# Performance work log

Measured on AMD Instinct MI355X. Metric: run time of the kernel, lower is better.

The kernel has to match this reference:

```python
import jax, jax.numpy as jnp
import numpy as np
from functools import partial

STRIDES = (8, 16, 32)
FMP = ((256, 256), (128, 128), (64, 64))  # H, W per level (img 2048, strides 8/16/32)
A = 3          # anchors per cell
C = 80         # num classes
TOPK = 1000    # per-level top-k
CONF = 0.05
NMS_T = 0.6
IMG = 2048.0   # max(img_h, img_w)
OFFSET = 1.0e5 # per-class box offset so cross-class IoU == 0

ANCHOR_SIZE = np.array([[[10, 13], [16, 30], [33, 23]],
                        [[30, 61], [62, 45], [59, 119]],
                        [[116, 90], [156, 198], [373, 326]]], np.float32)


def setup_inputs() -> dict:
    key = jax.random.key(0)
    ks = jax.random.split(key, 9)
    inp = {}
    for lvl, (h, w) in enumerate(FMP):
        m = h * w * A
        inp[f"obj{lvl}"] = jax.random.normal(ks[3 * lvl + 0], (m, 1), jnp.float32)
        inp[f"cls{lvl}"] = jax.random.normal(ks[3 * lvl + 1], (m, C), jnp.float32)
        inp[f"reg{lvl}"] = jax.random.normal(ks[3 * lvl + 2], (m, 4), jnp.float32)
    inp["anchor_size"] = jnp.asarray(ANCHOR_SIZE)
    return inp


def make_anchors(h, w, stride, a_size):
    # a_size: [A, 2]. Matches generate_anchors (cell centers * stride, tiled anchor wh).
    ys, xs = jnp.meshgrid(jnp.arange(h), jnp.arange(w), indexing="ij")
    xy = jnp.stack([xs, ys], -1).reshape(-1, 2).astype(jnp.float32) + 0.5  # [HW, 2]
    xy = jnp.repeat(xy, A, axis=0) * stride                                # [HW*A, 2]
    wh = jnp.tile(a_size, (h * w, 1))                                      # [HW*A, 2]
    return xy, wh


def decode_boxes(axy, awh, reg, stride):
    ctr = axy + (jax.nn.sigmoid(reg[..., :2]) * 3.0 - 1.5) * stride
    wh = jnp.exp(reg[..., 2:]) * awh
    return jnp.concatenate([ctr - 0.5 * wh, ctr + 0.5 * wh], axis=-1)


def iou_matrix(b):
    # b: [N, 4] xyxy
    area = (b[:, 2] - b[:, 0]) * (b[:, 3] - b[:, 1])
    lt = jnp.maximum(b[:, None, :2], b[None, :, :2])
    rb = jnp.minimum(b[:, None, 2:], b[None, :, 2:])
    whi = jnp.clip(rb - lt, 0.0)
    inter = whi[..., 0] * whi[..., 1]
    return inter / (area[:, None] + area[None, :] - inter + 1e-12)


def _post_process(levels, anchor_size):
    all_s, all_l, all_b = [], [], []
    for lvl, (obj, cls, reg) in enumerate(levels):
        h, w = FMP[lvl]
        stride = float(STRIDES[lvl])
        axy, awh = make_anchors(h, w, stride, anchor_size[lvl])
        # joint score, flattened over anchors x classes  -> [M*C]
        scores = jnp.sqrt(jax.nn.sigmoid(obj) * jax.nn.sigmoid(cls)).reshape(-1)
        topk_scores, topk_idx = jax.lax.top_k(scores, TOPK)
        anchor_idx = topk_idx // C
        labels = topk_idx % C
        boxes = decode_boxes(axy[anchor_idx], awh[anchor_idx], reg[anchor_idx], stride)
        # conf filter done by zeroing scores (fixed shapes under jit)
        topk_scores = jnp.where(topk_scores > CONF, topk_scores, 0.0)
        all_s.append(topk_scores); all_l.append(labels); all_b.append(boxes)
    scores = jnp.concatenate(all_s)   # [3*TOPK]
    labels = jnp.concatenate(all_l)
    boxes = jnp.concatenate(all_b)    # [3*TOPK, 4]

    n = scores.shape[0]
    # per-class NMS via class offset (cross-class IoU = 0), greedy over score order
    obox = boxes + labels.astype(boxes.dtype)[:, None] * OFFSET
    order = jnp.argsort(-scores)
    scores_s, labels_s, boxes_s = scores[order], labels[order], boxes[order]
    iou = iou_matrix(obox[order])

    def step(supp, i):
        keep_i = jnp.logical_and(~supp[i], scores_s[i] > CONF)
        supp = supp | (keep_i & (iou[i] > NMS_T) & (jnp.arange(n) > i))
        return supp, keep_i

    _, keep = jax.lax.scan(step, jnp.zeros(n, bool), jnp.arange(n))

    boxes_out = jnp.clip(boxes_s / IMG, 0.0, 1.0)
    scores_out = scores_s * keep.astype(scores_s.dtype)  # suppressed -> score 0
    return boxes_out, scores_out, labels_s


@jax.jit
def reference(obj0, cls0, reg0, obj1, cls1, reg1, obj2, cls2, reg2, anchor_size):
    levels = [(obj0, cls0, reg0), (obj1, cls1, reg1), (obj2, cls2, reg2)]
    return _post_process(levels, anchor_size)
```

## Files before the change

kernel.cpp:

```cpp
#include <hip/hip_runtime.h>
#include <stdint.h>
#include <math.h>

#pragma clang fp contract(off)

typedef unsigned int u32;
typedef unsigned long long u64;

#define M0 196608
#define M1 49152
#define M2 12288
#define MTOT (M0 + M1 + M2)
#define QCAP 8192
#define CCAP 524288
#define SCAP 2048
#define NSEL 3000
#define MASKW 48
#define NCH 47
#define FLOOR_BITS 0x3F4CCCCDu

__device__ __forceinline__ float sigf(float x) { return 1.0f / (1.0f + expf(-x)); }
__device__ __forceinline__ float sig_cr(float x) {
  float e = (float)exp(-(double)x);
  return 1.0f / (1.0f + e);
}

__device__ __forceinline__ void lvlmap(int b, int& lvl, u32& base, int& aoff) {
  if (b < 960)       { lvl = 0; base = (u32)b * 4096u;          aoff = 0; }
  else if (b < 1200) { lvl = 1; base = (u32)(b - 960) * 4096u;  aoff = M0; }
  else               { lvl = 2; base = (u32)(b - 1200) * 4096u; aoff = M0 + M1; }
}

__global__ void ksig_init(const float* __restrict__ o0, const float* __restrict__ o1,
                          const float* __restrict__ o2, float2* __restrict__ sopair,
                          u32* __restrict__ ghist, u32* __restrict__ qcnt,
                          u64* __restrict__ okbits, u64* __restrict__ nzbits) {
  int g = blockIdx.x * 256 + threadIdx.x;
  if (g < 6144) ghist[g] = 0u;
  if (g < 8) qcnt[g] = 0u;
  if (g < 64) { okbits[g] = 0ull; nzbits[g] = 0ull; }
  if (g >= MTOT) return;
  float x = (g < M0) ? o0[g] : (g < M0 + M1 ? o1[g - M0] : o2[g - M0 - M1]);
  float so = sigf(x);
  float tc;
  if (so <= 0.64f) tc = 3.0e38f;
  else {
    float r = 0.64f / so;
    tc = logf(r / (1.0f - r)) - 0.01f;
  }
  sopair[g] = make_float2(so, tc);
}

__global__ __launch_bounds__(256) void khist2(
    const float4* __restrict__ cls0, const float4* __restrict__ cls1,
    const float4* __restrict__ cls2, const float2* __restrict__ sopair,
    u32* __restrict__ ghist, u64* __restrict__ cand, u32* __restrict__ qcnt) {
  __shared__ u32 hist[2048];
  __shared__ u64 stage[SCAP];
  __shared__ u32 scount, gbase;
  int tid = threadIdx.x;
  for (int i = tid; i < 2048; i += 256) hist[i] = 0u;
  if (tid == 0) scount = 0u;
  __syncthreads();
  int lvl, aoff; u32 base;
  lvlmap(blockIdx.x, lvl, base, aoff);
  const float4* cls = lvl == 0 ? cls0 : (lvl == 1 ? cls1 : cls2);
#pragma unroll 4
  for (int c = 0; c < 16; c++) {
    u32 f4i = base + (u32)(c * 256 + tid);
    float4 v = cls[f4i];
    float2 sp = sopair[aoff + (int)(f4i / 20u)];
    float xs[4] = {v.x, v.y, v.z, v.w};
#pragma unroll
    for (int k = 0; k < 4; k++) {
      if (xs[k] >= sp.y) {
        u32 bits = __float_as_uint(sqrtf(sp.x * sigf(xs[k])));
        if (bits >= FLOOR_BITS) {
          atomicAdd(&hist[(bits - 0x3F000000u) >> 12], 1u);
          u32 sp_ = atomicAdd(&scount, 1u);
          if (sp_ < SCAP) {
            u32 idx = f4i * 4u + (u32)k;
            stage[sp_] = ((u64)__float_as_uint(xs[k]) << 32) |
                         ((u64)lvl << 24) | (u64)idx;
          }
        }
      }
    }
  }
  __syncthreads();
  u32 n = scount; if (n > SCAP) n = SCAP;
  if (tid == 0) {
    gbase = atomicAdd(&qcnt[3], n);
    if (scount > SCAP) atomicOr(&qcnt[4], 1u);
  }
  __syncthreads();
  u32 gb = gbase;
  for (u32 i = tid; i < n; i += 256) {
    u32 gp = gb + i;
    if (gp < CCAP) cand[gp] = stage[i];
    else if (i == 0) atomicOr(&qcnt[4], 1u);
  }
  for (int i = tid; i < 2048; i += 256) {
    u32 h = hist[i];
    if (h) atomicAdd(&ghist[lvl * 2048 + i], h);
  }
}

__global__ void kthresh(const u32* __restrict__ ghist, u32* __restrict__ thresh) {
  __shared__ u32 A[2048], Bb[2048];
  int lvl = blockIdx.x, tid = threadIdx.x;
  for (int i = tid; i < 2048; i += 256) A[i] = ghist[lvl * 2048 + i];
  __syncthreads();
  u32 *src = A, *dst = Bb;
  for (int off = 1; off < 2048; off <<= 1) {
    for (int i = tid; i < 2048; i += 256)
      dst[i] = src[i] + ((i + off < 2048) ? src[i + off] : 0u);
    __syncthreads();
    u32* t = src; src = dst; dst = t;
  }
  if (tid == 0 && src[0] < 1000u) thresh[lvl] = FLOOR_BITS;
  for (int i = tid; i < 2048; i += 256) {
    u32 S = src[i];
    u32 Sn = (i < 2047) ? src[i + 1] : 0u;
    if (S >= 1000u && Sn < 1000u) {
      u32 th = 0x3F000000u + ((u32)i << 12);
      thresh[lvl] = (th >= 0x3F000000u + 1024u) ? th - 1024u : 0x3F000000u;
    }
  }
}

__global__ __launch_bounds__(256) void kfilter(
    const u64* __restrict__ cand, const float2* __restrict__ sopair,
    const float* __restrict__ obj0, const float* __restrict__ obj1,
    const float* __restrict__ obj2, const u32* __restrict__ thresh,
    u32* __restrict__ qsc, u32* __restrict__ qidx, u32* __restrict__ qcnt) {
  if (qcnt[4] != 0u) return;
  u32 cnt = qcnt[3]; if (cnt > CCAP) cnt = CCAP;
  for (u32 i = blockIdx.x * 256u + threadIdx.x; i < cnt; i += 256u * 256u) {
    u64 e = cand[i];
    float clsv = __uint_as_float((u32)(e >> 32));
    u32 lo = (u32)e;
    int lvl = (int)((lo >> 24) & 3u);
    u32 idx = lo & 0xFFFFFFu;
    u32 anchor = idx / 80u;
    int aoff = lvl == 0 ? 0 : (lvl == 1 ? M0 : M0 + M1);
    float so = sopair[aoff + (int)anchor].x;
    u32 bits = __float_as_uint(sqrtf(so * sigf(clsv)));
    if (bits >= thresh[lvl]) {
      const float* obj = lvl == 0 ? obj0 : (lvl == 1 ? obj1 : obj2);
      float s = sqrtf(sig_cr(obj[anchor]) * sig_cr(clsv));
      u32 qp = atomicAdd(&qcnt[lvl], 1u);
      if (qp < QCAP) {
        qsc[lvl * QCAP + qp] = __float_as_uint(s);
        qidx[lvl * QCAP + qp] = idx;
      }
    }
  }
}

__global__ __launch_bounds__(256) void kqual_fb(
    const float4* __restrict__ cls0, const float4* __restrict__ cls1,
    const float4* __restrict__ cls2, const float2* __restrict__ sopair,
    const float* __restrict__ obj0, const float* __restrict__ obj1,
    const float* __restrict__ obj2, const u32* __restrict__ thresh,
    u32* __restrict__ qsc, u32* __restrict__ qidx, u32* __restrict__ qcnt) {
  if (qcnt[4] == 0u) return;
  int lvl, aoff; u32 base;
  lvlmap(blockIdx.x, lvl, base, aoff);
  const float4* cls = lvl == 0 ? cls0 : (lvl == 1 ? cls1 : cls2);
  const float* obj = lvl == 0 ? obj0 : (lvl == 1 ? obj1 : obj2);
  u32 th = thresh[lvl];
  int tid = threadIdx.x;
  for (int c = 0; c < 16; c++) {
    u32 f4i = base + (u32)(c * 256 + tid);
    float4 v = cls[f4i];
    float2 sp = sopair[aoff + (int)(f4i / 20u)];
    float xs[4] = {v.x, v.y, v.z, v.w};
#pragma unroll
    for (int k = 0; k < 4; k++) {
      if (xs[k] >= sp.y) {
        u32 bits = __float_as_uint(sqrtf(sp.x * sigf(xs[k])));
        if (bits >= th) {
          u32 idx = f4i * 4u + (u32)k;
          u32 anchor = idx / 80u;
          float s = sqrtf(sig_cr(obj[anchor]) * sig_cr(xs[k]));
          u32 qp = atomicAdd(&qcnt[lvl], 1u);
          if (qp < QCAP) {
            qsc[lvl * QCAP + qp] = __float_as_uint(s);
            qidx[lvl * QCAP + qp] = idx;
          }
        }
      }
    }
  }
}

__global__ __launch_bounds__(256) void krank(
    const u32* __restrict__ qsc, const u32* __restrict__ qidx,
    const u32* __restrict__ qcnt,
    const float4* __restrict__ reg0, const float4* __restrict__ reg1,
    const float4* __restrict__ reg2, const float* __restrict__ asz,
    u32* __restrict__ label_u, float4* __restrict__ box_u,
    float* __restrict__ lscore) {
  __shared__ u32 kb[2048];
  __shared__ u32 ki[2048];
  int lvl = blockIdx.x >> 5;
  int t = (blockIdx.x & 31) * 256 + threadIdx.x;
  u32 qn = qcnt[lvl]; if (qn > QCAP) qn = QCAP;
  u32 mb = 0, mi = 0; bool has = t < (int)qn;
  if (has) { mb = qsc[lvl * QCAP + t]; mi = qidx[lvl * QCAP + t]; }
  u32 rank = 0;
  for (u32 b0 = 0; b0 < qn; b0 += 2048u) {
    u32 m = qn - b0; if (m > 2048u) m = 2048u;
    u32 mpad = (m + 7u) & ~7u;
    __syncthreads();
    for (u32 j = threadIdx.x; j < mpad; j += 256) {
      if (j < m) { kb[j] = qsc[lvl * QCAP + b0 + j]; ki[j] = qidx[lvl * QCAP + b0 + j]; }
      else       { kb[j] = 0u; ki[j] = 0xFFFFFFFFu; }
    }
    __syncthreads();
    if (has) {
      u32 r0 = 0, r1 = 0, r2 = 0, r3 = 0;
      for (u32 j = 0; j < mpad; j += 8) {
        u32 a0 = kb[j+0], a1 = kb[j+1], a2 = kb[j+2], a3 = kb[j+3];
        u32 a4 = kb[j+4], a5 = kb[j+5], a6 = kb[j+6], a7 = kb[j+7];
        u32 i0 = ki[j+0], i1 = ki[j+1], i2 = ki[j+2], i3 = ki[j+3];
        u32 i4 = ki[j+4], i5 = ki[j+5], i6 = ki[j+6], i7 = ki[j+7];
        r0 += (a0 > mb || (a0 == mb && i0 < mi)) ? 1u : 0u;
        r1 += (a1 > mb || (a1 == mb && i1 < mi)) ? 1u : 0u;
        r2 += (a2 > mb || (a2 == mb && i2 < mi)) ? 1u : 0u;
        r3 += (a3 > mb || (a3 == mb && i3 < mi)) ? 1u : 0u;
        r0 += (a4 > mb || (a4 == mb && i4 < mi)) ? 1u : 0u;
        r1 += (a5 > mb || (a5 == mb && i5 < mi)) ? 1u : 0u;
        r2 += (a6 > mb || (a6 == mb && i6 < mi)) ? 1u : 0u;
        r3 += (a7 > mb || (a7 == mb && i7 < mi)) ? 1u : 0u;
      }
      rank += r0 + r1 + r2 + r3;
    }
  }
  if (!has || rank >= 1000u) return;

  int p = lvl * 1000 + (int)rank;
  u32 idx = mi;
  u32 anchor = idx / 80u;
  u32 label = idx - anchor * 80u;
  u32 cell = anchor / 3u;
  u32 a = anchor - cell * 3u;
  int W = 256 >> lvl;
  u32 x = cell & (u32)(W - 1);
  u32 y = cell >> (8 - lvl);
  float stride = (float)(8 << lvl);
  float ax = ((float)x + 0.5f) * stride;
  float ay = ((float)y + 0.5f) * stride;
  const float4* reg = lvl == 0 ? reg0 : (lvl == 1 ? reg1 : reg2);
  float4 rg = reg[anchor];
  float aw = asz[lvl * 6 + (int)a * 2 + 0];
  float ah = asz[lvl * 6 + (int)a * 2 + 1];
  float cx = ax + (sigf(rg.x) * 3.0f - 1.5f) * stride;
  float cy = ay + (sigf(rg.y) * 3.0f - 1.5f) * stride;
  float bw = expf(rg.z) * aw;
  float bh = expf(rg.w) * ah;
  box_u[p] = make_float4(cx - 0.5f * bw, cy - 0.5f * bh, cx + 0.5f * bw, cy + 0.5f * bh);
  label_u[p] = label;
  float sv = __uint_as_float(mb);
  lscore[p] = (sv > 0.05f) ? sv : 0.0f;
}

__device__ __forceinline__ u32 cnt_ge(const float* A, float s) {
  u32 lo = 0, hi = 1000;
  while (lo < hi) { u32 mid = (lo + hi) >> 1; if (A[mid] >= s) lo = mid + 1; else hi = mid; }
  return lo;
}
__device__ __forceinline__ u32 cnt_gt(const float* A, float s) {
  u32 lo = 0, hi = 1000;
  while (lo < hi) { u32 mid = (lo + hi) >> 1; if (A[mid] > s) lo = mid + 1; else hi = mid; }
  return lo;
}

__global__ __launch_bounds__(256) void kmerge(const float* __restrict__ lscore,
                                              const u32* __restrict__ label_u,
                                              const float4* __restrict__ box_u,
                                              float* __restrict__ sscore,
                                              float4* __restrict__ obox,
                                              u64* __restrict__ okbits,
                                              float* __restrict__ out) {
  __shared__ float s0[1000], s1[1000], s2[1000];
  int tid = threadIdx.x;
  for (int j = tid; j < 1000; j += 256) {
    s0[j] = lscore[j]; s1[j] = lscore[1000 + j]; s2[j] = lscore[2000 + j];
  }
  __syncthreads();
  int p = blockIdx.x * 256 + tid;
  if (p >= NSEL) return;
  int lvl = p / 1000, r = p - lvl * 1000;
  float s = lvl == 0 ? s0[r] : (lvl == 1 ? s1[r] : s2[r]);
  u32 rank = (u32)r;
  if (lvl == 0)      rank += cnt_gt(s1, s) + cnt_gt(s2, s);
  else if (lvl == 1) rank += cnt_ge(s0, s) + cnt_gt(s2, s);
  else               rank += cnt_ge(s0, s) + cnt_ge(s1, s);

  u32 label = label_u[p];
  float4 bx = box_u[p];
  sscore[rank] = s;
  float off = (float)label * 1.0e5f;
  obox[rank] = make_float4(bx.x + off, bx.y + off, bx.z + off, bx.w + off);
  out[rank * 4 + 0] = fminf(fmaxf(bx.x / 2048.0f, 0.0f), 1.0f);
  out[rank * 4 + 1] = fminf(fmaxf(bx.y / 2048.0f, 0.0f), 1.0f);
  out[rank * 4 + 2] = fminf(fmaxf(bx.z / 2048.0f, 0.0f), 1.0f);
  out[rank * 4 + 3] = fminf(fmaxf(bx.w / 2048.0f, 0.0f), 1.0f);
  out[15000 + rank] = (float)label;
  if (s > 0.05f) atomicOr(&okbits[rank >> 6], 1ull << (rank & 63));
}

__global__ __launch_bounds__(256) void kiou(const float4* __restrict__ obox,
                                            u64* __restrict__ mask,
                                            u64* __restrict__ diag,
                                            u64* __restrict__ nzbits) {
  __shared__ u32 crossflags;
  int tid = threadIdx.x;
  if (tid == 0) crossflags = 0u;
  __syncthreads();
  int i0 = blockIdx.x * 4;
  float4 b0v = obox[i0 + 0], b1v = obox[i0 + 1], b2v = obox[i0 + 2], b3v = obox[i0 + 3];
  float a0 = (b0v.z - b0v.x) * (b0v.w - b0v.y);
  float a1 = (b1v.z - b1v.x) * (b1v.w - b1v.y);
  float a2 = (b2v.z - b2v.x) * (b2v.w - b2v.y);
  float a3 = (b3v.z - b3v.x) * (b3v.w - b3v.y);
  bool c0 = false, c1 = false, c2 = false, c3 = false;
  for (int it = 0; it < 12; it++) {
    int jj = it * 256 + tid;
    int jc = jj < NSEL ? jj : NSEL - 1;
    float4 bj = obox[jc];
    float aj = (bj.z - bj.x) * (bj.w - bj.y);
    int wi = it * 4 + (tid >> 6);
#define DOROW(R, BV, AV, CV) do {                                              \
      float ltx = fmaxf(BV.x, bj.x), lty = fmaxf(BV.y, bj.y);                  \
      float rbx = fminf(BV.z, bj.z), rby = fminf(BV.w, bj.w);                  \
      float ww = fmaxf(rbx - ltx, 0.0f), hh = fmaxf(rby - lty, 0.0f);          \
      float inter = ww * hh;                                                   \
      float iou = inter / (((AV + aj) - inter) + 1e-12f);                      \
      bool cond = (jj < NSEL) && (jj > (i0 + R)) && (iou > 0.6f);              \
      CV |= (cond && wi != ((i0 + R) >> 6));                                   \
      u64 m = __ballot(cond);                                                  \
      if ((tid & 63) == 0) {                                                   \
        mask[(u64)(i0 + R) * MASKW + (u64)wi] = m;                             \
        if (wi == ((i0 + R) >> 6)) diag[i0 + R] = m;                           \
      }                                                                        \
    } while (0)
    DOROW(0, b0v, a0, c0); DOROW(1, b1v, a1, c1);
    DOROW(2, b2v, a2, c2); DOROW(3, b3v, a3, c3);
#undef DOROW
  }
  u64 bb;
  bb = __ballot(c0); if ((tid & 63) == 0 && bb) atomicOr(&crossflags, 1u);
  bb = __ballot(c1); if ((tid & 63) == 0 && bb) atomicOr(&crossflags, 2u);
  bb = __ballot(c2); if ((tid & 63) == 0 && bb) atomicOr(&crossflags, 4u);
  bb = __ballot(c3); if ((tid & 63) == 0 && bb) atomicOr(&crossflags, 8u);
  __syncthreads();
  if (tid < 4 && ((crossflags >> tid) & 1u))
    atomicOr(&nzbits[(i0 + tid) >> 6], 1ull << ((i0 + tid) & 63));
}

__global__ __launch_bounds__(64) void knms(const u64* __restrict__ mask,
                                           const u64* __restrict__ diag,
                                           const u64* __restrict__ okbits,
                                           const u64* __restrict__ nzbits,
                                           const float* __restrict__ sscore,
                                           float* __restrict__ out) {
  __shared__ u64 sdiag[NCH * 64];
  __shared__ float ssc[NCH * 64];
  int l = threadIdx.x;
  for (int i = l; i < NCH * 64; i += 64) {
    sdiag[i] = (i < NSEL) ? diag[i] : 0ull;
    ssc[i]   = (i < NSEL) ? sscore[i] : 0.0f;
  }
  u64 okw_l = (l < NCH) ? okbits[l] : 0ull;
  u64 nz_l  = (l < NCH) ? nzbits[l] : 0ull;
  u64 supp = 0ull;
  __syncthreads();
  for (int c = 0; c < NCH; c++) {
    int base = c * 64;
    u64 cur = __shfl(supp, c);
    u64 okw = __shfl(okw_l, c);
    u64 nzw = __shfl(nz_l, c);
    u64 dj = sdiag[base + l];
    u64 diagnz = __ballot(dj != 0ull);
    u64 avail = okw & ~cur;
    u64 isupp = 0ull, procd = 0ull, tent = avail;
    while (true) {
      tent = avail & ~isupp;
      u64 evs = tent & diagnz & ~procd;
      if (evs == 0ull) break;
      int j = __ffsll((long long)evs) - 1;
      procd |= (1ull << j);
      isupp |= __shfl(dj, j);
    }
    u64 kept = tent;
    int row = base + l;
    if (row < NSEL) out[12000 + row] = ((kept >> l) & 1ull) ? ssc[row] : 0.0f;
    u64 orrows = kept & nzw;
    while (orrows) {
      int j = __ffsll((long long)orrows) - 1;
      orrows &= orrows - 1ull;
      u64 w = (l < NCH) ? mask[(u64)(base + j) * MASKW + l] : 0ull;
      supp |= w;
    }
  }
}

extern "C" void kernel_launch(void* const* d_in, const int* in_sizes, int n_in,
                              void* d_out, int out_size, void* d_ws, size_t ws_size,
                              hipStream_t stream) {
  const float* obj0 = (const float*)d_in[0];
  const float* cls0 = (const float*)d_in[1];
  const float* reg0 = (const float*)d_in[2];
  const float* obj1 = (const float*)d_in[3];
  const float* cls1 = (const float*)d_in[4];
  const float* reg1 = (const float*)d_in[5];
  const float* obj2 = (const float*)d_in[6];
  const float* cls2 = (const float*)d_in[7];
  const float* reg2 = (const float*)d_in[8];
  const float* asz  = (const float*)d_in[9];
  float* out = (float*)d_out;

  char* wsp = (char*)d_ws;
  size_t off = 0;
  auto alloc = [&](size_t bytes) -> void* {
    void* p = wsp + off;
    off += (bytes + 255) & ~(size_t)255;
    return p;
  };
  float2* sopair = (float2*)alloc((size_t)MTOT * 8);
  u32* ghist   = (u32*)alloc((size_t)3 * 2048 * 4);
  u32* qcnt    = (u32*)alloc(64);
  u32* thresh  = (u32*)alloc(64);
  u64* cand    = (u64*)alloc((size_t)CCAP * 8);
  u32* qsc     = (u32*)alloc((size_t)3 * QCAP * 4);
  u32* qidx    = (u32*)alloc((size_t)3 * QCAP * 4);
  u32* label_u = (u32*)alloc((size_t)NSEL * 4);
  float4* box_u  = (float4*)alloc((size_t)NSEL * 16);
  float* lscore  = (float*)alloc((size_t)NSEL * 4);
  float4* obox   = (float4*)alloc((size_t)NSEL * 16);
  float* sscore  = (float*)alloc((size_t)NSEL * 4);
  u64* okbits    = (u64*)alloc(64 * 8);
  u64* nzbits    = (u64*)alloc(64 * 8);
  u64* diag      = (u64*)alloc((size_t)NSEL * 8);
  u64* mask      = (u64*)alloc((size_t)NSEL * MASKW * 8);
  if (off > ws_size) return;

  ksig_init<<<dim3(1008), dim3(256), 0, stream>>>(obj0, obj1, obj2, sopair,
                                                  ghist, qcnt, okbits, nzbits);
  khist2<<<dim3(1260), dim3(256), 0, stream>>>((const float4*)cls0, (const float4*)cls1,
                                               (const float4*)cls2, sopair, ghist,
                                               cand, qcnt);
  kthresh<<<dim3(3), dim3(256), 0, stream>>>(ghist, thresh);
  kfilter<<<dim3(256), dim3(256), 0, stream>>>(cand, sopair, obj0, obj1, obj2,
                                               thresh, qsc, qidx, qcnt);
  kqual_fb<<<dim3(1260), dim3(256), 0, stream>>>((const float4*)cls0, (const float4*)cls1,
                                                 (const float4*)cls2, sopair,
                                                 obj0, obj1, obj2, thresh,
                                                 qsc, qidx, qcnt);
  krank<<<dim3(96), dim3(256), 0, stream>>>(qsc, qidx, qcnt, (const float4*)reg0,
                                            (const float4*)reg1, (const float4*)reg2,
                                            asz, label_u, box_u, lscore);
  kmerge<<<dim3(12), dim3(256), 0, stream>>>(lscore, label_u, box_u, sscore, obox,
                                             okbits, out);
  kiou<<<dim3(750), dim3(256), 0, stream>>>(obox, mask, diag, nzbits);
  knms<<<dim3(1), dim3(64), 0, stream>>>(mask, diag, okbits, nzbits, sscore, out);
}
```

Baseline: 280.5 us.

## Fuse post-histogram stages into one cooperative kernel and drop sigmoid precompute

Replaces the sequence of small tail kernels (threshold, filter, fallback, rank, merge, IoU, NMS) with a single cooperative kernel that uses grid-wide syncs between phases. The objectness-sigmoid precompute kernel is removed by computing per-anchor sigmoid and threshold in shared memory inside the histogram kernel, which also gains a per-float4 max early-out. Candidates now store score bits instead of raw logits. Workspace clearing moves to a memset. The aim is to cut launch gaps and the extra global pass, at the cost of grid-sync overhead and a fixed 256-block tail.

```diff
diff --git a/kernel.cpp b/kernel.cpp
--- a/kernel.cpp
+++ b/kernel.cpp
@@ -1,8 +1,11 @@
 #include <hip/hip_runtime.h>
+#include <hip/hip_cooperative_groups.h>
 #include <stdint.h>
 #include <math.h>
 
 #pragma clang fp contract(off)
+
+namespace cg = cooperative_groups;
 
 typedef unsigned int u32;
 typedef unsigned long long u64;
@@ -10,14 +13,16 @@
 #define M0 196608
 #define M1 49152
 #define M2 12288
-#define MTOT (M0 + M1 + M2)
 #define QCAP 8192
 #define CCAP 524288
-#define SCAP 2048
+#define SCAP 1024
+#define FSTG 256
 #define NSEL 3000
 #define MASKW 48
 #define NCH 47
 #define FLOOR_BITS 0x3F4CCCCDu
+#define NBLK_H 2520
+#define TBLK 256
 
 __device__ __forceinline__ float sigf(float x) { return 1.0f / (1.0f + expf(-x)); }
 __device__ __forceinline__ float sig_cr(float x) {
@@ -25,63 +30,59 @@
   return 1.0f / (1.0f + e);
 }
 
-__device__ __forceinline__ void lvlmap(int b, int& lvl, u32& base, int& aoff) {
-  if (b < 960)       { lvl = 0; base = (u32)b * 4096u;          aoff = 0; }
-  else if (b < 1200) { lvl = 1; base = (u32)(b - 960) * 4096u;  aoff = M0; }
-  else               { lvl = 2; base = (u32)(b - 1200) * 4096u; aoff = M0 + M1; }
-}
-
-__global__ void ksig_init(const float* __restrict__ o0, const float* __restrict__ o1,
-                          const float* __restrict__ o2, float2* __restrict__ sopair,
-                          u32* __restrict__ ghist, u32* __restrict__ qcnt,
-                          u64* __restrict__ okbits, u64* __restrict__ nzbits) {
-  int g = blockIdx.x * 256 + threadIdx.x;
-  if (g < 6144) ghist[g] = 0u;
-  if (g < 8) qcnt[g] = 0u;
-  if (g < 64) { okbits[g] = 0ull; nzbits[g] = 0ull; }
-  if (g >= MTOT) return;
-  float x = (g < M0) ? o0[g] : (g < M0 + M1 ? o1[g - M0] : o2[g - M0 - M1]);
-  float so = sigf(x);
-  float tc;
-  if (so <= 0.64f) tc = 3.0e38f;
-  else {
-    float r = 0.64f / so;
-    tc = logf(r / (1.0f - r)) - 0.01f;
-  }
-  sopair[g] = make_float2(so, tc);
+__device__ __forceinline__ void lvlmap2(int b, int& lvl, u32& base) {
+  if (b < 1920)      { lvl = 0; base = (u32)b * 2048u; }
+  else if (b < 2400) { lvl = 1; base = (u32)(b - 1920) * 2048u; }
+  else               { lvl = 2; base = (u32)(b - 2400) * 2048u; }
 }
 
 __global__ __launch_bounds__(256) void khist2(
     const float4* __restrict__ cls0, const float4* __restrict__ cls1,
-    const float4* __restrict__ cls2, const float2* __restrict__ sopair,
+    const float4* __restrict__ cls2, const float* __restrict__ obj0,
+    const float* __restrict__ obj1, const float* __restrict__ obj2,
     u32* __restrict__ ghist, u64* __restrict__ cand, u32* __restrict__ qcnt) {
   __shared__ u32 hist[2048];
   __shared__ u64 stage[SCAP];
+  __shared__ float sof[112], tcf[112];
   __shared__ u32 scount, gbase;
   int tid = threadIdx.x;
   for (int i = tid; i < 2048; i += 256) hist[i] = 0u;
   if (tid == 0) scount = 0u;
+  int lvl; u32 base;
+  lvlmap2(blockIdx.x, lvl, base);
+  const float4* cls = lvl == 0 ? cls0 : (lvl == 1 ? cls1 : cls2);
+  const float* obj = lvl == 0 ? obj0 : (lvl == 1 ? obj1 : obj2);
+  u32 a0 = base / 20u;
+  u32 na = (base + 2047u) / 20u - a0 + 1u;
+  if (tid < (int)na) {
+    float so = sigf(obj[a0 + tid]);
+    float tc;
+    if (so <= 0.64f) tc = 3.0e38f;
+    else { float r = 0.64f / so; tc = logf(r / (1.0f - r)) - 0.01f; }
+    sof[tid] = so; tcf[tid] = tc;
+  }
   __syncthreads();
-  int lvl, aoff; u32 base;
-  lvlmap(blockIdx.x, lvl, base, aoff);
-  const float4* cls = lvl == 0 ? cls0 : (lvl == 1 ? cls1 : cls2);
-#pragma unroll 4
-  for (int c = 0; c < 16; c++) {
+#pragma unroll 2
+  for (int c = 0; c < 8; c++) {
     u32 f4i = base + (u32)(c * 256 + tid);
     float4 v = cls[f4i];
-    float2 sp = sopair[aoff + (int)(f4i / 20u)];
-    float xs[4] = {v.x, v.y, v.z, v.w};
+    u32 ai = f4i / 20u - a0;
+    float tc = tcf[ai];
+    float mx = fmaxf(fmaxf(v.x, v.y), fmaxf(v.z, v.w));
+    if (mx >= tc) {
+      float so = sof[ai];
+      float xs[4] = {v.x, v.y, v.z, v.w};
 #pragma unroll
-    for (int k = 0; k < 4; k++) {
-      if (xs[k] >= sp.y) {
-        u32 bits = __float_as_uint(sqrtf(sp.x * sigf(xs[k])));
-        if (bits >= FLOOR_BITS) {
-          atomicAdd(&hist[(bits - 0x3F000000u) >> 12], 1u);
-          u32 sp_ = atomicAdd(&scount, 1u);
-          if (sp_ < SCAP) {
-            u32 idx = f4i * 4u + (u32)k;
-            stage[sp_] = ((u64)__float_as_uint(xs[k]) << 32) |
-                         ((u64)lvl << 24) | (u64)idx;
+      for (int k = 0; k < 4; k++) {
+        if (xs[k] >= tc) {
+          u32 bits = __float_as_uint(sqrtf(so * sigf(xs[k])));
+          if (bits >= FLOOR_BITS) {
+            atomicAdd(&hist[(bits - 0x3F000000u) >> 12], 1u);
+            u32 sp = atomicAdd(&scount, 1u);
+            if (sp < SCAP) {
+              u32 idx = f4i * 4u + (u32)k;
+              stage[sp] = ((u64)bits << 32) | ((u64)lvl << 24) | (u64)idx;
+            }
           }
         }
       }
@@ -91,14 +92,13 @@
   u32 n = scount; if (n > SCAP) n = SCAP;
   if (tid == 0) {
     gbase = atomicAdd(&qcnt[3], n);
-    if (scount > SCAP) atomicOr(&qcnt[4], 1u);
+    if (scount > SCAP || gbase + n > CCAP) atomicOr(&qcnt[4], 1u);
   }
   __syncthreads();
   u32 gb = gbase;
   for (u32 i = tid; i < n; i += 256) {
     u32 gp = gb + i;
     if (gp < CCAP) cand[gp] = stage[i];
-    else if (i == 0) atomicOr(&qcnt[4], 1u);
   }
   for (int i = tid; i < 2048; i += 256) {
     u32 h = hist[i];
@@ -106,165 +106,29 @@
   }
 }
 
-__global__ void kthresh(const u32* __restrict__ ghist, u32* __restrict__ thresh) {
-  __shared__ u32 A[2048], Bb[2048];
-  int lvl = blockIdx.x, tid = threadIdx.x;
-  for (int i = tid; i < 2048; i += 256) A[i] = ghist[lvl * 2048 + i];
-  __syncthreads();
-  u32 *src = A, *dst = Bb;
-  for (int off = 1; off < 2048; off <<= 1) {
-    for (int i = tid; i < 2048; i += 256)
-      dst[i] = src[i] + ((i + off < 2048) ? src[i + off] : 0u);
-    __syncthreads();
-    u32* t = src; src = dst; dst = t;
-  }
-  if (tid == 0 && src[0] < 1000u) thresh[lvl] = FLOOR_BITS;
-  for (int i = tid; i < 2048; i += 256) {
-    u32 S = src[i];
-    u32 Sn = (i < 2047) ? src[i + 1] : 0u;
-    if (S >= 1000u && Sn < 1000u) {
-      u32 th = 0x3F000000u + ((u32)i << 12);
-      thresh[lvl] = (th >= 0x3F000000u + 1024u) ? th - 1024u : 0x3F000000u;
-    }
-  }
-}
-
-__global__ __launch_bounds__(256) void kfilter(
-    const u64* __restrict__ cand, const float2* __restrict__ sopair,
-    const float* __restrict__ obj0, const float* __restrict__ obj1,
-    const float* __restrict__ obj2, const u32* __restrict__ thresh,
-    u32* __restrict__ qsc, u32* __restrict__ qidx, u32* __restrict__ qcnt) {
-  if (qcnt[4] != 0u) return;
-  u32 cnt = qcnt[3]; if (cnt > CCAP) cnt = CCAP;
-  for (u32 i = blockIdx.x * 256u + threadIdx.x; i < cnt; i += 256u * 256u) {
-    u64 e = cand[i];
-    float clsv = __uint_as_float((u32)(e >> 32));
-    u32 lo = (u32)e;
-    int lvl = (int)((lo >> 24) & 3u);
-    u32 idx = lo & 0xFFFFFFu;
-    u32 anchor = idx / 80u;
-    int aoff = lvl == 0 ? 0 : (lvl == 1 ? M0 : M0 + M1);
-    float so = sopair[aoff + (int)anchor].x;
-    u32 bits = __float_as_uint(sqrtf(so * sigf(clsv)));
-    if (bits >= thresh[lvl]) {
-      const float* obj = lvl == 0 ? obj0 : (lvl == 1 ? obj1 : obj2);
-      float s = sqrtf(sig_cr(obj[anchor]) * sig_cr(clsv));
-      u32 qp = atomicAdd(&qcnt[lvl], 1u);
-      if (qp < QCAP) {
-        qsc[lvl * QCAP + qp] = __float_as_uint(s);
-        qidx[lvl * QCAP + qp] = idx;
-      }
-    }
-  }
-}
-
-__global__ __launch_bounds__(256) void kqual_fb(
-    const float4* __restrict__ cls0, const float4* __restrict__ cls1,
-    const float4* __restrict__ cls2, const float2* __restrict__ sopair,
-    const float* __restrict__ obj0, const float* __restrict__ obj1,
-    const float* __restrict__ obj2, const u32* __restrict__ thresh,
-    u32* __restrict__ qsc, u32* __restrict__ qidx, u32* __restrict__ qcnt) {
-  if (qcnt[4] == 0u) return;
-  int lvl, aoff; u32 base;
-  lvlmap(blockIdx.x, lvl, base, aoff);
-  const float4* cls = lvl == 0 ? cls0 : (lvl == 1 ? cls1 : cls2);
-  const float* obj = lvl == 0 ? obj0 : (lvl == 1 ? obj1 : obj2);
-  u32 th = thresh[lvl];
-  int tid = threadIdx.x;
-  for (int c = 0; c < 16; c++) {
-    u32 f4i = base + (u32)(c * 256 + tid);
-    float4 v = cls[f4i];
-    float2 sp = sopair[aoff + (int)(f4i / 20u)];
-    float xs[4] = {v.x, v.y, v.z, v.w};
-#pragma unroll
-    for (int k = 0; k < 4; k++) {
-      if (xs[k] >= sp.y) {
-        u32 bits = __float_as_uint(sqrtf(sp.x * sigf(xs[k])));
-        if (bits >= th) {
-          u32 idx = f4i * 4u + (u32)k;
-          u32 anchor = idx / 80u;
-          float s = sqrtf(sig_cr(obj[anchor]) * sig_cr(xs[k]));
-          u32 qp = atomicAdd(&qcnt[lvl], 1u);
-          if (qp < QCAP) {
-            qsc[lvl * QCAP + qp] = __float_as_uint(s);
-            qidx[lvl * QCAP + qp] = idx;
-          }
-        }
-      }
-    }
-  }
-}
-
-__global__ __launch_bounds__(256) void krank(
-    const u32* __restrict__ qsc, const u32* __restrict__ qidx,
-    const u32* __restrict__ qcnt,
-    const float4* __restrict__ reg0, const float4* __restrict__ reg1,
-    const float4* __restrict__ reg2, const float* __restrict__ asz,
-    u32* __restrict__ label_u, float4* __restrict__ box_u,
-    float* __restrict__ lscore) {
-  __shared__ u32 kb[2048];
-  __shared__ u32 ki[2048];
-  int lvl = blockIdx.x >> 5;
-  int t = (blockIdx.x & 31) * 256 + threadIdx.x;
-  u32 qn = qcnt[lvl]; if (qn > QCAP) qn = QCAP;
-  u32 mb = 0, mi = 0; bool has = t < (int)qn;
-  if (has) { mb = qsc[lvl * QCAP + t]; mi = qidx[lvl * QCAP + t]; }
-  u32 rank = 0;
-  for (u32 b0 = 0; b0 < qn; b0 += 2048u) {
-    u32 m = qn - b0; if (m > 2048u) m = 2048u;
-    u32 mpad = (m + 7u) & ~7u;
-    __syncthreads();
-    for (u32 j = threadIdx.x; j < mpad; j += 256) {
-      if (j < m) { kb[j] = qsc[lvl * QCAP + b0 + j]; ki[j] = qidx[lvl * QCAP + b0 + j]; }
-      else       { kb[j] = 0u; ki[j] = 0xFFFFFFFFu; }
-    }
-    __syncthreads();
-    if (has) {
-      u32 r0 = 0, r1 = 0, r2 = 0, r3 = 0;
-      for (u32 j = 0; j < mpad; j += 8) {
-        u32 a0 = kb[j+0], a1 = kb[j+1], a2 = kb[j+2], a3 = kb[j+3];
-        u32 a4 = kb[j+4], a5 = kb[j+5], a6 = kb[j+6], a7 = kb[j+7];
-        u32 i0 = ki[j+0], i1 = ki[j+1], i2 = ki[j+2], i3 = ki[j+3];
-        u32 i4 = ki[j+4], i5 = ki[j+5], i6 = ki[j+6], i7 = ki[j+7];
-        r0 += (a0 > mb || (a0 == mb && i0 < mi)) ? 1u : 0u;
-        r1 += (a1 > mb || (a1 == mb && i1 < mi)) ? 1u : 0u;
-        r2 += (a2 > mb || (a2 == mb && i2 < mi)) ? 1u : 0u;
-        r3 += (a3 > mb || (a3 == mb && i3 < mi)) ? 1u : 0u;
-        r0 += (a4 > mb || (a4 == mb && i4 < mi)) ? 1u : 0u;
-        r1 += (a5 > mb || (a5 == mb && i5 < mi)) ? 1u : 0u;
-        r2 += (a6 > mb || (a6 == mb && i6 < mi)) ? 1u : 0u;
-        r3 += (a7 > mb || (a7 == mb && i7 < mi)) ? 1u : 0u;
-      }
-      rank += r0 + r1 + r2 + r3;
-    }
-  }
-  if (!has || rank >= 1000u) return;
-
-  int p = lvl * 1000 + (int)rank;
-  u32 idx = mi;
-  u32 anchor = idx / 80u;
-  u32 label = idx - anchor * 80u;
-  u32 cell = anchor / 3u;
-  u32 a = anchor - cell * 3u;
-  int W = 256 >> lvl;
-  u32 x = cell & (u32)(W - 1);
-  u32 y = cell >> (8 - lvl);
-  float stride = (float)(8 << lvl);
-  float ax = ((float)x + 0.5f) * stride;
-  float ay = ((float)y + 0.5f) * stride;
-  const float4* reg = lvl == 0 ? reg0 : (lvl == 1 ? reg1 : reg2);
-  float4 rg = reg[anchor];
-  float aw = asz[lvl * 6 + (int)a * 2 + 0];
-  float ah = asz[lvl * 6 + (int)a * 2 + 1];
-  float cx = ax + (sigf(rg.x) * 3.0f - 1.5f) * stride;
-  float cy = ay + (sigf(rg.y) * 3.0f - 1.5f) * stride;
-  float bw = expf(rg.z) * aw;
-  float bh = expf(rg.w) * ah;
-  box_u[p] = make_float4(cx - 0.5f * bw, cy - 0.5f * bh, cx + 0.5f * bw, cy + 0.5f * bh);
-  label_u[p] = label;
-  float sv = __uint_as_float(mb);
-  lscore[p] = (sv > 0.05f) ? sv : 0.0f;
-}
+struct TailArgs {
+  const float *obj0, *obj1, *obj2;
+  const float *cls0f, *cls1f, *cls2f;
+  const float4 *cls0, *cls1, *cls2;
+  const float4 *reg0, *reg1, *reg2;
+  const float *asz;
+  u32 *ghist, *qcnt, *thresh;
+  u64 *cand;
+  u32 *qsc, *qidx, *label_u;
+  float4 *box_u;
+  float *lscore;
+  float4 *obox;
+  float *sscore;
+  u64 *okbits, *nzbits, *diag, *mask;
+  float *out;
+};
+
+struct SmemA { u32 A[2048]; u32 B[2048]; };
+struct SmemB { u32 sc[3][FSTG]; u32 si[3][FSTG]; u32 cnt[3]; u32 gb[3]; };
+struct SmemC { u32 kb[2048]; u32 ki[2048]; };
+struct SmemD { float s0[1000], s1[1000], s2[1000]; u64 okb[NCH]; };
+struct SmemF { u64 sdiag[NCH * 64]; float ssc[NCH * 64]; };
+union TailSmem { SmemA a; SmemB b; SmemC c; SmemD d; SmemF f; };
 
 __device__ __forceinline__ u32 cnt_ge(const float* A, float s) {
   u32 lo = 0, hi = 1000;
@@ -277,133 +141,290 @@
   return lo;
 }
 
-__global__ __launch_bounds__(256) void kmerge(const float* __restrict__ lscore,
-                                              const u32* __restrict__ label_u,
-                                              const float4* __restrict__ box_u,
-                                              float* __restrict__ sscore,
-                                              float4* __restrict__ obox,
-                                              u64* __restrict__ okbits,
-                                              float* __restrict__ out) {
-  __shared__ float s0[1000], s1[1000], s2[1000];
+__global__ __launch_bounds__(256) void ktail(TailArgs ta) {
+  cg::grid_group grid = cg::this_grid();
+  __shared__ TailSmem sm;
+  int bid = blockIdx.x;
   int tid = threadIdx.x;
-  for (int j = tid; j < 1000; j += 256) {
-    s0[j] = lscore[j]; s1[j] = lscore[1000 + j]; s2[j] = lscore[2000 + j];
-  }
-  __syncthreads();
-  int p = blockIdx.x * 256 + tid;
-  if (p >= NSEL) return;
-  int lvl = p / 1000, r = p - lvl * 1000;
-  float s = lvl == 0 ? s0[r] : (lvl == 1 ? s1[r] : s2[r]);
-  u32 rank = (u32)r;
-  if (lvl == 0)      rank += cnt_gt(s1, s) + cnt_gt(s2, s);
-  else if (lvl == 1) rank += cnt_ge(s0, s) + cnt_gt(s2, s);
-  else               rank += cnt_ge(s0, s) + cnt_ge(s1, s);
-
-  u32 label = label_u[p];
-  float4 bx = box_u[p];
-  sscore[rank] = s;
-  float off = (float)label * 1.0e5f;
-  obox[rank] = make_float4(bx.x + off, bx.y + off, bx.z + off, bx.w + off);
-  out[rank * 4 + 0] = fminf(fmaxf(bx.x / 2048.0f, 0.0f), 1.0f);
-  out[rank * 4 + 1] = fminf(fmaxf(bx.y / 2048.0f, 0.0f), 1.0f);
-  out[rank * 4 + 2] = fminf(fmaxf(bx.z / 2048.0f, 0.0f), 1.0f);
-  out[rank * 4 + 3] = fminf(fmaxf(bx.w / 2048.0f, 0.0f), 1.0f);
-  out[15000 + rank] = (float)label;
-  if (s > 0.05f) atomicOr(&okbits[rank >> 6], 1ull << (rank & 63));
-}
-
-__global__ __launch_bounds__(256) void kiou(const float4* __restrict__ obox,
-                                            u64* __restrict__ mask,
-                                            u64* __restrict__ diag,
-                                            u64* __restrict__ nzbits) {
-  __shared__ u32 crossflags;
-  int tid = threadIdx.x;
-  if (tid == 0) crossflags = 0u;
-  __syncthreads();
-  int i0 = blockIdx.x * 4;
-  float4 b0v = obox[i0 + 0], b1v = obox[i0 + 1], b2v = obox[i0 + 2], b3v = obox[i0 + 3];
-  float a0 = (b0v.z - b0v.x) * (b0v.w - b0v.y);
-  float a1 = (b1v.z - b1v.x) * (b1v.w - b1v.y);
-  float a2 = (b2v.z - b2v.x) * (b2v.w - b2v.y);
-  float a3 = (b3v.z - b3v.x) * (b3v.w - b3v.y);
-  bool c0 = false, c1 = false, c2 = false, c3 = false;
-  for (int it = 0; it < 12; it++) {
-    int jj = it * 256 + tid;
-    int jc = jj < NSEL ? jj : NSEL - 1;
-    float4 bj = obox[jc];
-    float aj = (bj.z - bj.x) * (bj.w - bj.y);
-    int wi = it * 4 + (tid >> 6);
+
+  if (bid < 3) {
+    int lvl = bid;
+    if (tid == 0) ta.thresh[lvl] = FLOOR_BITS;
+    for (int i = tid; i < 2048; i += 256) sm.a.A[i] = ta.ghist[lvl * 2048 + i];
+    __syncthreads();
+    u32 *src = sm.a.A, *dst = sm.a.B;
+    for (int off = 1; off < 2048; off <<= 1) {
+      for (int i = tid; i < 2048; i += 256)
+        dst[i] = src[i] + ((i + off < 2048) ? src[i + off] : 0u);
+      __syncthreads();
+      u32* t = src; src = dst; dst = t;
+    }
+    for (int i = tid; i < 2048; i += 256) {
+      u32 S = src[i];
+      u32 Sn = (i < 2047) ? src[i + 1] : 0u;
+      if (S >= 1000u && Sn < 1000u) {
+        u32 th = 0x3F000000u + ((u32)i << 12);
+        ta.thresh[lvl] = (th >= 0x3F000000u + 1024u) ? th - 1024u : 0x3F000000u;
+      }
+    }
+  }
+  grid.sync();
+
+  if (ta.qcnt[4] == 0u) {
+    if (tid < 3) sm.b.cnt[tid] = 0u;
+    __syncthreads();
+    u32 cnt = ta.qcnt[3]; if (cnt > CCAP) cnt = CCAP;
+    u32 th0 = ta.thresh[0], th1 = ta.thresh[1], th2 = ta.thresh[2];
+    for (u32 i = (u32)(bid * 256 + tid); i < cnt; i += (u32)TBLK * 256u) {
+      u64 e = ta.cand[i];
+      u32 bits = (u32)(e >> 32);
+      int lvl = (int)((e >> 24) & 3u);
+      u32 idx = (u32)e & 0xFFFFFFu;
+      u32 th = lvl == 0 ? th0 : (lvl == 1 ? th1 : th2);
+      if (bits >= th) {
+        const float* obj = lvl == 0 ? ta.obj0 : (lvl == 1 ? ta.obj1 : ta.obj2);
+        const float* clsf = lvl == 0 ? ta.cls0f : (lvl == 1 ? ta.cls1f : ta.cls2f);
+        u32 anchor = idx / 80u;
+        float s = sqrtf(sig_cr(obj[anchor]) * sig_cr(clsf[idx]));
+        u32 p = atomicAdd(&sm.b.cnt[lvl], 1u);
+        if (p < FSTG) { sm.b.sc[lvl][p] = __float_as_uint(s); sm.b.si[lvl][p] = idx; }
+        else {
+          u32 qp = atomicAdd(&ta.qcnt[lvl], 1u);
+          if (qp < QCAP) { ta.qsc[lvl * QCAP + qp] = __float_as_uint(s);
+                           ta.qidx[lvl * QCAP + qp] = idx; }
+        }
+      }
+    }
+    __syncthreads();
+    for (int l = 0; l < 3; l++) {
+      u32 n = sm.b.cnt[l]; if (n > FSTG) n = FSTG;
+      if (tid == 0) sm.b.gb[l] = atomicAdd(&ta.qcnt[l], n);
+      __syncthreads();
+      u32 g = sm.b.gb[l];
+      for (u32 i = tid; i < n; i += 256) {
+        u32 qp = g + i;
+        if (qp < QCAP) { ta.qsc[l * QCAP + qp] = sm.b.sc[l][i];
+                         ta.qidx[l * QCAP + qp] = sm.b.si[l][i]; }
+      }
+      __syncthreads();
+    }
+  } else {
+    for (int vb = bid; vb < NBLK_H; vb += TBLK) {
+      int lvl; u32 base;
+      lvlmap2(vb, lvl, base);
+      const float4* cls = lvl == 0 ? ta.cls0 : (lvl == 1 ? ta.cls1 : ta.cls2);
+      const float* obj = lvl == 0 ? ta.obj0 : (lvl == 1 ? ta.obj1 : ta.obj2);
+      u32 th = ta.thresh[lvl];
+      for (int c = 0; c < 8; c++) {
+        u32 f4i = base + (u32)(c * 256 + tid);
+        float4 v = cls[f4i];
+        u32 anchor = f4i / 20u;
+        float so = sigf(obj[anchor]);
+        float xs[4] = {v.x, v.y, v.z, v.w};
+#pragma unroll
+        for (int k = 0; k < 4; k++) {
+          u32 bits = __float_as_uint(sqrtf(so * sigf(xs[k])));
+          if (bits >= th) {
+            u32 idx = f4i * 4u + (u32)k;
+            float s = sqrtf(sig_cr(obj[anchor]) * sig_cr(xs[k]));
+            u32 qp = atomicAdd(&ta.qcnt[lvl], 1u);
+            if (qp < QCAP) { ta.qsc[lvl * QCAP + qp] = __float_as_uint(s);
+                             ta.qidx[lvl * QCAP + qp] = idx; }
+          }
+        }
+      }
+    }
+  }
+  grid.sync();
+
+  if (bid < 96) {
+    int lvl = bid >> 5;
+    int t = (bid & 31) * 256 + tid;
+    u32 qn = ta.qcnt[lvl]; if (qn > QCAP) qn = QCAP;
+    u32 mb = 0, mi = 0; bool has = t < (int)qn;
+    if (has) { mb = ta.qsc[lvl * QCAP + t]; mi = ta.qidx[lvl * QCAP + t]; }
+    u32 rank = 0;
+    for (u32 b0 = 0; b0 < qn; b0 += 2048u) {
+      u32 m = qn - b0; if (m > 2048u) m = 2048u;
+      u32 mpad = (m + 7u) & ~7u;
+      __syncthreads();
+      for (u32 j = tid; j < mpad; j += 256) {
+        if (j < m) { sm.c.kb[j] = ta.qsc[lvl * QCAP + b0 + j];
+                     sm.c.ki[j] = ta.qidx[lvl * QCAP + b0 + j]; }
+        else       { sm.c.kb[j] = 0u; sm.c.ki[j] = 0xFFFFFFFFu; }
+      }
+      __syncthreads();
+      if (has) {
+        u32 r0 = 0, r1 = 0, r2 = 0, r3 = 0;
+        for (u32 j = 0; j < mpad; j += 8) {
+          u32 a0 = sm.c.kb[j+0], a1 = sm.c.kb[j+1], a2 = sm.c.kb[j+2], a3 = sm.c.kb[j+3];
+          u32 a4 = sm.c.kb[j+4], a5 = sm.c.kb[j+5], a6 = sm.c.kb[j+6], a7 = sm.c.kb[j+7];
+          u32 i0 = sm.c.ki[j+0], i1 = sm.c.ki[j+1], i2 = sm.c.ki[j+2], i3 = sm.c.ki[j+3];
+          u32 i4 = sm.c.ki[j+4], i5 = sm.c.ki[j+5], i6 = sm.c.ki[j+6], i7 = sm.c.ki[j+7];
+          r0 += (a0 > mb || (a0 == mb && i0 < mi)) ? 1u : 0u;
+          r1 += (a1 > mb || (a1 == mb && i1 < mi)) ? 1u : 0u;
+          r2 += (a2 > mb || (a2 == mb && i2 < mi)) ? 1u : 0u;
+          r3 += (a3 > mb || (a3 == mb && i3 < mi)) ? 1u : 0u;
+          r0 += (a4 > mb || (a4 == mb && i4 < mi)) ? 1u : 0u;
+          r1 += (a5 > mb || (a5 == mb && i5 < mi)) ? 1u : 0u;
+          r2 += (a6 > mb || (a6 == mb && i6 < mi)) ? 1u : 0u;
+          r3 += (a7 > mb || (a7 == mb && i7 < mi)) ? 1u : 0u;
+        }
+        rank += r0 + r1 + r2 + r3;
+      }
+    }
+    if (has && rank < 1000u) {
+      int p = lvl * 1000 + (int)rank;
+      u32 idx = mi;
+      u32 anchor = idx / 80u;
+      u32 label = idx - anchor * 80u;
+      u32 cell = anchor / 3u;
+      u32 a = anchor - cell * 3u;
+      int W = 256 >> lvl;
+      u32 x = cell & (u32)(W - 1);
+      u32 y = cell >> (8 - lvl);
+      float stride = (float)(8 << lvl);
+      float ax = ((float)x + 0.5f) * stride;
+      float ay = ((float)y + 0.5f) * stride;
+      const float4* reg = lvl == 0 ? ta.reg0 : (lvl == 1 ? ta.reg1 : ta.reg2);
+      float4 rg = reg[anchor];
+      float aw = ta.asz[lvl * 6 + (int)a * 2 + 0];
+      float ah = ta.asz[lvl * 6 + (int)a * 2 + 1];
+      float cx = ax + (sigf(rg.x) * 3.0f - 1.5f) * stride;
+      float cy = ay + (sigf(rg.y) * 3.0f - 1.5f) * stride;
+      float bw = expf(rg.z) * aw;
+      float bh = expf(rg.w) * ah;
+      ta.box_u[p] = make_float4(cx - 0.5f * bw, cy - 0.5f * bh,
+                                cx + 0.5f * bw, cy + 0.5f * bh);
+      ta.label_u[p] = label;
+      float sv = __uint_as_float(mb);
+      ta.lscore[p] = (sv > 0.05f) ? sv : 0.0f;
+    }
+  }
+  grid.sync();
+
+  if (bid < 12) {
+    for (int j = tid; j < 1000; j += 256) {
+      sm.d.s0[j] = ta.lscore[j];
+      sm.d.s1[j] = ta.lscore[1000 + j];
+      sm.d.s2[j] = ta.lscore[2000 + j];
+    }
+    for (int j = tid; j < NCH; j += 256) sm.d.okb[j] = 0ull;
+    __syncthreads();
+    int p = bid * 256 + tid;
+    if (p < NSEL) {
+      int lvl = p / 1000, r = p - lvl * 1000;
+      float s = lvl == 0 ? sm.d.s0[r] : (lvl == 1 ? sm.d.s1[r] : sm.d.s2[r]);
+      u32 rank = (u32)r;
+      if (lvl == 0)      rank += cnt_gt(sm.d.s1, s) + cnt_gt(sm.d.s2, s);
+      else if (lvl == 1) rank += cnt_ge(sm.d.s0, s) + cnt_gt(sm.d.s2, s);
+      else               rank += cnt_ge(sm.d.s0, s) + cnt_ge(sm.d.s1, s);
+      u32 label = ta.label_u[p];
+      float4 bx = ta.box_u[p];
+      ta.sscore[rank] = s;
+      float off = (float)label * 1.0e5f;
+      ta.obox[rank] = make_float4(bx.x + off, bx.y + off, bx.z + off, bx.w + off);
+      ta.out[rank * 4 + 0] = fminf(fmaxf(bx.x / 2048.0f, 0.0f), 1.0f);
+      ta.out[rank * 4 + 1] = fminf(fmaxf(bx.y / 2048.0f, 0.0f), 1.0f);
+      ta.out[rank * 4 + 2] = fminf(fmaxf(bx.z / 2048.0f, 0.0f), 1.0f);
+      ta.out[rank * 4 + 3] = fminf(fmaxf(bx.w / 2048.0f, 0.0f), 1.0f);
+      ta.out[15000 + rank] = (float)label;
+      if (s > 0.05f) atomicOr(&sm.d.okb[rank >> 6], 1ull << (rank & 63));
+    }
+    __syncthreads();
+    for (int j = tid; j < NCH; j += 256) {
+      u64 w = sm.d.okb[j];
+      if (w) atomicOr(&ta.okbits[j], w);
+    }
+  }
+  grid.sync();
+
+  for (int g = 0; g < 3; g++) {
+    int i0 = bid * 12 + g * 4;
+    if (i0 < NSEL) {
+      float4 b0v = ta.obox[i0 + 0], b1v = ta.obox[i0 + 1];
+      float4 b2v = ta.obox[i0 + 2], b3v = ta.obox[i0 + 3];
+      float a0 = (b0v.z - b0v.x) * (b0v.w - b0v.y);
+      float a1 = (b1v.z - b1v.x) * (b1v.w - b1v.y);
+      float a2 = (b2v.z - b2v.x) * (b2v.w - b2v.y);
+      float a3 = (b3v.z - b3v.x) * (b3v.w - b3v.y);
+      bool c0 = false, c1 = false, c2 = false, c3 = false;
+      for (int it = 0; it < 12; it++) {
+        int jj = it * 256 + tid;
+        int jc = jj < NSEL ? jj : NSEL - 1;
+        float4 bj = ta.obox[jc];
+        float aj = (bj.z - bj.x) * (bj.w - bj.y);
+        int wi = it * 4 + (tid >> 6);
 #define DOROW(R, BV, AV, CV) do {                                              \
-      float ltx = fmaxf(BV.x, bj.x), lty = fmaxf(BV.y, bj.y);                  \
-      float rbx = fminf(BV.z, bj.z), rby = fminf(BV.w, bj.w);                  \
-      float ww = fmaxf(rbx - ltx, 0.0f), hh = fmaxf(rby - lty, 0.0f);          \
-      float inter = ww * hh;                                                   \
-      float iou = inter / (((AV + aj) - inter) + 1e-12f);                      \
-      bool cond = (jj < NSEL) && (jj > (i0 + R)) && (iou > 0.6f);              \
-      CV |= (cond && wi != ((i0 + R) >> 6));                                   \
-      u64 m = __ballot(cond);                                                  \
-      if ((tid & 63) == 0) {                                                   \
-        mask[(u64)(i0 + R) * MASKW + (u64)wi] = m;                             \
-        if (wi == ((i0 + R) >> 6)) diag[i0 + R] = m;                           \
-      }                                                                        \
-    } while (0)
-    DOROW(0, b0v, a0, c0); DOROW(1, b1v, a1, c1);
-    DOROW(2, b2v, a2, c2); DOROW(3, b3v, a3, c3);
+        float ltx = fmaxf(BV.x, bj.x), lty = fmaxf(BV.y, bj.y);                \
+        float rbx = fminf(BV.z, bj.z), rby = fminf(BV.w, bj.w);                \
+        float ww = fmaxf(rbx - ltx, 0.0f), hh = fmaxf(rby - lty, 0.0f);        \
+        float inter = ww * hh;                                                 \
+        float iou = inter / (((AV + aj) - inter) + 1e-12f);                    \
+        bool cond = (jj < NSEL) && (jj > (i0 + R)) && (iou > 0.6f);            \
+        CV |= (cond && wi != ((i0 + R) >> 6));                                 \
+        u64 m = __ballot(cond);                                                \
+        if ((tid & 63) == 0) {                                                 \
+          ta.mask[(u64)(i0 + R) * MASKW + (u64)wi] = m;                        \
+          if (wi == ((i0 + R) >> 6)) ta.diag[i0 + R] = m;                      \
+        }                                                                      \
+      } while (0)
+        DOROW(0, b0v, a0, c0); DOROW(1, b1v, a1, c1);
+        DOROW(2, b2v, a2, c2); DOROW(3, b3v, a3, c3);
 #undef DOROW
-  }
-  u64 bb;
-  bb = __ballot(c0); if ((tid & 63) == 0 && bb) atomicOr(&crossflags, 1u);
-  bb = __ballot(c1); if ((tid & 63) == 0 && bb) atomicOr(&crossflags, 2u);
-  bb = __ballot(c2); if ((tid & 63) == 0 && bb) atomicOr(&crossflags, 4u);
-  bb = __ballot(c3); if ((tid & 63) == 0 && bb) atomicOr(&crossflags, 8u);
-  __syncthreads();
-  if (tid < 4 && ((crossflags >> tid) & 1u))
-    atomicOr(&nzbits[(i0 + tid) >> 6], 1ull << ((i0 + tid) & 63));
-}
-
-__global__ __launch_bounds__(64) void knms(const u64* __restrict__ mask,
-                                           const u64* __restrict__ diag,
-                                           const u64* __restrict__ okbits,
-                                           const u64* __restrict__ nzbits,
-                                           const float* __restrict__ sscore,
-                                           float* __restrict__ out) {
-  __shared__ u64 sdiag[NCH * 64];
-  __shared__ float ssc[NCH * 64];
-  int l = threadIdx.x;
-  for (int i = l; i < NCH * 64; i += 64) {
-    sdiag[i] = (i < NSEL) ? diag[i] : 0ull;
-    ssc[i]   = (i < NSEL) ? sscore[i] : 0.0f;
-  }
-  u64 okw_l = (l < NCH) ? okbits[l] : 0ull;
-  u64 nz_l  = (l < NCH) ? nzbits[l] : 0ull;
-  u64 supp = 0ull;
-  __syncthreads();
-  for (int c = 0; c < NCH; c++) {
-    int base = c * 64;
-    u64 cur = __shfl(supp, c);
-    u64 okw = __shfl(okw_l, c);
-    u64 nzw = __shfl(nz_l, c);
-    u64 dj = sdiag[base + l];
-    u64 diagnz = __ballot(dj != 0ull);
-    u64 avail = okw & ~cur;
-    u64 isupp = 0ull, procd = 0ull, tent = avail;
-    while (true) {
-      tent = avail & ~isupp;
-      u64 evs = tent & diagnz & ~procd;
-      if (evs == 0ull) break;
-      int j = __ffsll((long long)evs) - 1;
-      procd |= (1ull << j);
-      isupp |= __shfl(dj, j);
-    }
-    u64 kept = tent;
-    int row = base + l;
-    if (row < NSEL) out[12000 + row] = ((kept >> l) & 1ull) ? ssc[row] : 0.0f;
-    u64 orrows = kept & nzw;
-    while (orrows) {
-      int j = __ffsll((long long)orrows) - 1;
-      orrows &= orrows - 1ull;
-      u64 w = (l < NCH) ? mask[(u64)(base + j) * MASKW + l] : 0ull;
-      supp |= w;
+      }
+      u64 bb;
+      bb = __ballot(c0);
+      if ((tid & 63) == 0 && bb) atomicOr(&ta.nzbits[(i0 + 0) >> 6], 1ull << ((i0 + 0) & 63));
+      bb = __ballot(c1);
+      if ((tid & 63) == 0 && bb) atomicOr(&ta.nzbits[(i0 + 1) >> 6], 1ull << ((i0 + 1) & 63));
+      bb = __ballot(c2);
+      if ((tid & 63) == 0 && bb) atomicOr(&ta.nzbits[(i0 + 2) >> 6], 1ull << ((i0 + 2) & 63));
+      bb = __ballot(c3);
+      if ((tid & 63) == 0 && bb) atomicOr(&ta.nzbits[(i0 + 3) >> 6], 1ull << ((i0 + 3) & 63));
+    }
+  }
+  grid.sync();
+
+  if (bid == 0) {
+    for (int i = tid; i < NCH * 64; i += 256) {
+      sm.f.sdiag[i] = (i < NSEL) ? ta.diag[i] : 0ull;
+      sm.f.ssc[i]   = (i < NSEL) ? ta.sscore[i] : 0.0f;
+    }
+    __syncthreads();
+    if (tid < 64) {
+      int l = tid;
+      u64 okw_l = (l < NCH) ? ta.okbits[l] : 0ull;
+      u64 nz_l  = (l < NCH) ? ta.nzbits[l] : 0ull;
+      u64 supp = 0ull;
+      for (int c = 0; c < NCH; c++) {
+        int base = c * 64;
+        u64 cur = __shfl(supp, c);
+        u64 okw = __shfl(okw_l, c);
+        u64 nzw = __shfl(nz_l, c);
+        u64 dj = sm.f.sdiag[base + l];
+        u64 diagnz = __ballot(dj != 0ull);
+        u64 avail = okw & ~cur;
+        u64 isupp = 0ull, procd = 0ull, tent = avail;
+        while (true) {
+          tent = avail & ~isupp;
+          u64 evs = tent & diagnz & ~procd;
+          if (evs == 0ull) break;
+          int j = __ffsll((long long)evs) - 1;
+          procd |= (1ull << j);
+          isupp |= __shfl(dj, j);
+        }
+        u64 kept = tent;
+        int row = base + l;
+        if (row < NSEL) ta.out[12000 + row] = ((kept >> l) & 1ull) ? sm.f.ssc[row] : 0.0f;
+        u64 orrows = kept & nzw;
+        while (orrows) {
+          int j = __ffsll((long long)orrows) - 1;
+          orrows &= orrows - 1ull;
+          u64 w = (l < NCH) ? ta.mask[(u64)(base + j) * MASKW + l] : 0ull;
+          supp |= w;
+        }
+      }
     }
   }
 }
@@ -430,41 +451,45 @@
     off += (bytes + 255) & ~(size_t)255;
     return p;
   };
-  float2* sopair = (float2*)alloc((size_t)MTOT * 8);
-  u32* ghist   = (u32*)alloc((size_t)3 * 2048 * 4);
-  u32* qcnt    = (u32*)alloc(64);
-  u32* thresh  = (u32*)alloc(64);
-  u64* cand    = (u64*)alloc((size_t)CCAP * 8);
-  u32* qsc     = (u32*)alloc((size_t)3 * QCAP * 4);
-  u32* qidx    = (u32*)alloc((size_t)3 * QCAP * 4);
+  size_t z0 = off;
+  u32* ghist  = (u32*)alloc((size_t)3 * 2048 * 4);
+  u32* qcnt   = (u32*)alloc(64);
+  u64* okbits = (u64*)alloc(64 * 8);
+  u64* nzbits = (u64*)alloc(64 * 8);
+  size_t z1 = off;
+  u32* thresh = (u32*)alloc(64);
+  u64* cand   = (u64*)alloc((size_t)CCAP * 8);
+  u32* qsc    = (u32*)alloc((size_t)3 * QCAP * 4);
+  u32* qidx   = (u32*)alloc((size_t)3 * QCAP * 4);
   u32* label_u = (u32*)alloc((size_t)NSEL * 4);
   float4* box_u  = (float4*)alloc((size_t)NSEL * 16);
   float* lscore  = (float*)alloc((size_t)NSEL * 4);
   float4* obox   = (float4*)alloc((size_t)NSEL * 16);
   float* sscore  = (float*)alloc((size_t)NSEL * 4);
-  u64* okbits    = (u64*)alloc(64 * 8);
-  u64* nzbits    = (u64*)alloc(64 * 8);
   u64* diag      = (u64*)alloc((size_t)NSEL * 8);
   u64* mask      = (u64*)alloc((size_t)NSEL * MASKW * 8);
   if (off > ws_size) return;
 
-  ksig_init<<<dim3(1008), dim3(256), 0, stream>>>(obj0, obj1, obj2, sopair,
-                                                  ghist, qcnt, okbits, nzbits);
-  khist2<<<dim3(1260), dim3(256), 0, stream>>>((const float4*)cls0, (const float4*)cls1,
-                                               (const float4*)cls2, sopair, ghist,
-                                               cand, qcnt);
-  kthresh<<<dim3(3), dim3(256), 0, stream>>>(ghist, thresh);
-  kfilter<<<dim3(256), dim3(256), 0, stream>>>(cand, sopair, obj0, obj1, obj2,
-                                               thresh, qsc, qidx, qcnt);
-  kqual_fb<<<dim3(1260), dim3(256), 0, stream>>>((const float4*)cls0, (const float4*)cls1,
-                                                 (const float4*)cls2, sopair,
-                                                 obj0, obj1, obj2, thresh,
-                                                 qsc, qidx, qcnt);
-  krank<<<dim3(96), dim3(256), 0, stream>>>(qsc, qidx, qcnt, (const float4*)reg0,
-                                            (const float4*)reg1, (const float4*)reg2,
-                                            asz, label_u, box_u, lscore);
-  kmerge<<<dim3(12), dim3(256), 0, stream>>>(lscore, label_u, box_u, sscore, obox,
-                                             okbits, out);
-  kiou<<<dim3(750), dim3(256), 0, stream>>>(obox, mask, diag, nzbits);
-  knms<<<dim3(1), dim3(64), 0, stream>>>(mask, diag, okbits, nzbits, sscore, out);
-}
+  hipMemsetAsync(wsp + z0, 0, z1 - z0, stream);
+
+  khist2<<<dim3(NBLK_H), dim3(256), 0, stream>>>(
+      (const float4*)cls0, (const float4*)cls1, (const float4*)cls2,
+      obj0, obj1, obj2, ghist, cand, qcnt);
+
+  TailArgs ta;
+  ta.obj0 = obj0; ta.obj1 = obj1; ta.obj2 = obj2;
+  ta.cls0f = cls0; ta.cls1f = cls1; ta.cls2f = cls2;
+  ta.cls0 = (const float4*)cls0; ta.cls1 = (const float4*)cls1;
+  ta.cls2 = (const float4*)cls2;
+  ta.reg0 = (const float4*)reg0; ta.reg1 = (const float4*)reg1;
+  ta.reg2 = (const float4*)reg2;
+  ta.asz = asz;
+  ta.ghist = ghist; ta.qcnt = qcnt; ta.thresh = thresh;
+  ta.cand = cand; ta.qsc = qsc; ta.qidx = qidx;
+  ta.label_u = label_u; ta.box_u = box_u; ta.lscore = lscore;
+  ta.obox = obox; ta.sscore = sscore;
+  ta.okbits = okbits; ta.nzbits = nzbits; ta.diag = diag; ta.mask = mask;
+  ta.out = out;
+  void* kargs[] = { &ta };
+  hipLaunchCooperativeKernel((void*)ktail, dim3(TBLK), dim3(256), kargs, 0, stream);
+}
```

Measured after the change: 392.5 us. 39.9% more time.
